# Kernel tuning notes

Hardware: AMD Instinct MI355X
Metric: run time of the kernel (lower is better)

Reference implementation:

```python
import jax, jax.numpy as jnp
import numpy as np

# ---- MUSIC hyperparameters (from init_kwargs) ----
N_FFT = 512
HOP = 256
FS = 16000
F_LOW = 400
F_HIGH = 1000
D_INTER = 0.1
C_SOUND = 343.0
SOURCE_NUM = 2
MIC_NUM = 4
RESOLUTION = 0.01
EST_NUM = 4      # snapshots used for spatial covariance
T_START = 120    # starting STFT frame
EPS = 1e-8
N_SAMPLES = 9_600_000

# sqrt of periodic Hann window (torch.hann_window(512).pow(0.5))
_WIN = np.sqrt(0.5 * (1.0 - np.cos(2.0 * np.pi * np.arange(N_FFT) / N_FFT))).astype(np.float32)
# analog frequency grid and static usable-bin mask
_F_ALL = np.linspace(0.0, FS / 2.0, N_FFT // 2 + 1)
_F_MASK = (_F_ALL >= F_LOW) & (_F_ALL < F_HIGH)
_F_USE = _F_ALL[_F_MASK].astype(np.float32)          # (F_use,) ~ 19 bins
_N_ANGLES = int(180 / RESOLUTION + 1)                 # 18001


def setup_inputs() -> dict:
    key = jax.random.key(0)
    x = jax.random.normal(key, (N_SAMPLES, MIC_NUM), dtype=jnp.float32)
    return {"x": x}


def _music(x):
    # x: (T_samples, C) -> multichannel STFT, center=True reflect pad (torch.stft default)
    xc = x.T                                              # (C, T)
    pad = jnp.pad(xc, ((0, 0), (N_FFT // 2, N_FFT // 2)), mode="reflect")
    n_frames = 1 + x.shape[0] // HOP
    idx = np.arange(n_frames)[:, None] * HOP + np.arange(N_FFT)  # (Tf, 512)
    frames = pad[:, idx] * jnp.asarray(_WIN)              # (C, Tf, 512)
    X = jnp.fft.rfft(frames, axis=-1)                     # (C, Tf, 257) complex64
    X = X[:, :, _F_MASK]                                  # (C, Tf, F_use)

    # spatial covariance from EST_NUM snapshots starting at T_START
    Xs = X[:, T_START:T_START + EST_NUM, :]               # (C, est, F)
    spt = jnp.einsum("ctf,dtf->fcd", Xs, jnp.conj(Xs)) / EST_NUM  # (F, C, C) Hermitian

    # noise subspace: eigenvectors of the MIC_NUM - SOURCE_NUM smallest eigenvalues
    _, V = jnp.linalg.eigh(spt)                           # ascending eigenvalues
    En = V[:, :, : MIC_NUM - SOURCE_NUM]                  # (F, C, K)

    # steering vectors for all angles at once (vectorized over the 18001-angle loop)
    theta = jnp.deg2rad(jnp.linspace(-90.0, 90.0, _N_ANGLES))
    sin_t = jnp.sin(theta).astype(jnp.float32)            # (A,)
    mic_idx = jnp.arange(MIC_NUM, dtype=jnp.float32)      # (C,)
    f_use = jnp.asarray(_F_USE)                           # (F,)
    phase = (2.0 * jnp.pi * D_INTER / C_SOUND) * sin_t[:, None, None] \
            * f_use[None, :, None] * mic_idx[None, None, :]        # (A, F, C)
    steer = jnp.exp(-1j * phase)                          # (A, F, C) complex64

    # project onto noise subspace: MUSIC pseudo-spectrum
    proj = jnp.einsum("afc,fck->afk", steer, En)          # (A, F, K)
    denom = jnp.sum(jnp.abs(proj) ** 2, axis=-1) + EPS    # (A, F)
    spt_spec = jnp.mean(1.0 / denom, axis=1)              # mean over freqs -> (A,)
    return spt_spec


def reference(x):
    return _music(x)
```

## Files before the change

kernel.cpp:

```cpp
#include <hip/hip_runtime.h>
#include <math.h>

#define HOP 256
#define T_START 120
#define NFREQ 19
#define KMIN 13
#define NANGLES 18001

__constant__ double C8[8] = {1.0, 0.70710678118654752, 0.0, -0.70710678118654752,
                             -1.0, -0.70710678118654752, 0.0, 0.70710678118654752};
__constant__ double S8[8] = {0.0, 0.70710678118654752, 1.0, 0.70710678118654752,
                             0.0, -0.70710678118654752, -1.0, -0.70710678118654752};

__global__ __launch_bounds__(64) void k_dft(const float4* __restrict__ x4,
                                            double* __restrict__ ws) {
    const int blk  = blockIdx.x;
    const int k    = blk >> 2;
    const int t    = blk & 3;
    const int lane = threadIdx.x;
    const int kact = KMIN + k;
    const int base = (T_START - 1 + t) * HOP;

    const double cw8 = 0.92387953251128675613;
    const double sw8 = 0.38268343236508977173;
    double sw, cw;
    sincospi((double)lane / 512.0, &sw, &cw);

    double sp, cp;
    sincospi((double)(kact * lane) / 256.0, &sp, &cp);
    const int m = kact & 7;
    const double cd = C8[m], sd = S8[m];

    double xr0 = 0, xi0 = 0, xr1 = 0, xi1 = 0;
    double xr2 = 0, xi2 = 0, xr3 = 0, xi3 = 0;
#pragma unroll
    for (int j = 0; j < 8; ++j) {
        const float4 v = x4[base + lane + 64 * j];
        const double wr = sw * cp;
        const double wi = sw * sp;
        xr0 += (double)v.x * wr;  xi0 -= (double)v.x * wi;
        xr1 += (double)v.y * wr;  xi1 -= (double)v.y * wi;
        xr2 += (double)v.z * wr;  xi2 -= (double)v.z * wi;
        xr3 += (double)v.w * wr;  xi3 -= (double)v.w * wi;
        const double nw = sw * cw8 + cw * sw8;
        cw = cw * cw8 - sw * sw8;
        sw = nw;
        const double np = sp * cd + cp * sd;
        cp = cp * cd - sp * sd;
        sp = np;
    }
#pragma unroll
    for (int off = 32; off > 0; off >>= 1) {
        xr0 += __shfl_down(xr0, off, 64);  xi0 += __shfl_down(xi0, off, 64);
        xr1 += __shfl_down(xr1, off, 64);  xi1 += __shfl_down(xi1, off, 64);
        xr2 += __shfl_down(xr2, off, 64);  xi2 += __shfl_down(xi2, off, 64);
        xr3 += __shfl_down(xr3, off, 64);  xi3 += __shfl_down(xi3, off, 64);
    }
    if (lane == 0) {
        const int idx = k * 16 + t * 4;
        ws[2 * (idx + 0)] = xr0;  ws[2 * (idx + 0) + 1] = xi0;
        ws[2 * (idx + 1)] = xr1;  ws[2 * (idx + 1) + 1] = xi1;
        ws[2 * (idx + 2)] = xr2;  ws[2 * (idx + 2) + 1] = xi2;
        ws[2 * (idx + 3)] = xr3;  ws[2 * (idx + 3) + 1] = xi3;
    }
}

__global__ __launch_bounds__(256, 1) void k_eig_scan(const double* __restrict__ wsX,
                                                     float* __restrict__ out) {
    __shared__ double tb[NFREQ * 7];
    const int tid = threadIdx.x;
    const int i   = blockIdx.x * 256 + tid;

    const double deg = -90.0 + 0.01 * (double)i;
    const double sth = sin(deg * (M_PI / 180.0));
    const double KC  = 2.0 * M_PI * 0.1 / 343.0;
    const double a   = KC * sth;
    double c0, s0, cd, sd;
    sincos(a * (31.25 * (double)KMIN), &s0, &c0);
    sincos(a * 31.25, &sd, &cd);

    if (tid < NFREQ) {
        const int f = tid;
        double Xr[4][4], Xi[4][4];
#pragma unroll
        for (int t = 0; t < 4; ++t)
#pragma unroll
            for (int c = 0; c < 4; ++c) {
                const int idx = f * 16 + t * 4 + c;
                Xr[t][c] = wsX[2 * idx];
                Xi[t][c] = wsX[2 * idx + 1];
            }

        double Ar[4][4], Ai[4][4], Vr[4][4], Vi[4][4];
#pragma unroll
        for (int aa = 0; aa < 4; ++aa)
#pragma unroll
            for (int dd = 0; dd < 4; ++dd) {
                double ar = 0.0, ai = 0.0;
#pragma unroll
                for (int t = 0; t < 4; ++t) {
                    ar += Xr[t][aa] * Xr[t][dd] + Xi[t][aa] * Xi[t][dd];
                    ai += Xi[t][aa] * Xr[t][dd] - Xr[t][aa] * Xi[t][dd];
                }
                Ar[aa][dd] = 0.25 * ar;
                Ai[aa][dd] = 0.25 * ai;
                Vr[aa][dd] = (aa == dd) ? 1.0 : 0.0;
                Vi[aa][dd] = 0.0;
            }

        const int PP[6] = {0, 2, 0, 1, 0, 1};
        const int QQ[6] = {1, 3, 2, 3, 3, 2};
        for (int sweep = 0; sweep < 5; ++sweep) {
#pragma unroll
            for (int r6 = 0; r6 < 6; ++r6) {
                const int p = PP[r6], q = QQ[r6];
                const double zr = Ar[p][q], zi = Ai[p][q];
                const double rr = sqrt(zr * zr + zi * zi);
                if (rr < 1e-30) continue;
                const double tau = (Ar[q][q] - Ar[p][p]) / (2.0 * rr);
                const double sq  = sqrt(tau * tau + 1.0);
                const double tt  = (tau >= 0.0) ? (-1.0 / (tau + sq)) : (1.0 / (sq - tau));
                const double cc  = 1.0 / sqrt(1.0 + tt * tt);
                const double sg  = tt * cc;
                const double inv_r = 1.0 / rr;
                const double sr =  sg * zr * inv_r;
                const double si = -sg * zi * inv_r;
#pragma unroll
                for (int kk = 0; kk < 4; ++kk) {
                    const double apr = Ar[kk][p], api = Ai[kk][p];
                    const double aqr = Ar[kk][q], aqi = Ai[kk][q];
                    Ar[kk][p] = cc * apr + sr * aqr - si * aqi;
                    Ai[kk][p] = cc * api + sr * aqi + si * aqr;
                    Ar[kk][q] = cc * aqr - (sr * apr + si * api);
                    Ai[kk][q] = cc * aqi - (sr * api - si * apr);
                }
#pragma unroll
                for (int kk = 0; kk < 4; ++kk) {
                    const double apr = Ar[p][kk], api = Ai[p][kk];
                    const double aqr = Ar[q][kk], aqi = Ai[q][kk];
                    Ar[p][kk] = cc * apr + sr * aqr + si * aqi;
                    Ai[p][kk] = cc * api + sr * aqi - si * aqr;
                    Ar[q][kk] = cc * aqr - (sr * apr - si * api);
                    Ai[q][kk] = cc * aqi - (sr * api + si * apr);
                }
#pragma unroll
                for (int kk = 0; kk < 4; ++kk) {
                    const double vpr = Vr[kk][p], vpi = Vi[kk][p];
                    const double vqr = Vr[kk][q], vqi = Vi[kk][q];
                    Vr[kk][p] = cc * vpr + sr * vqr - si * vqi;
                    Vi[kk][p] = cc * vpi + sr * vqi + si * vqr;
                    Vr[kk][q] = cc * vqr - (sr * vpr + si * vpi);
                    Vi[kk][q] = cc * vqi - (sr * vpi - si * vpr);
                }
            }
        }

        double dg[4] = {Ar[0][0], Ar[1][1], Ar[2][2], Ar[3][3]};
        int i0 = 0;
#pragma unroll
        for (int j = 1; j < 4; ++j)
            if (dg[j] < dg[i0]) i0 = j;
        int i1 = (i0 == 0) ? 1 : 0;
#pragma unroll
        for (int j = 0; j < 4; ++j)
            if (j != i0 && dg[j] < dg[i1]) i1 = j;

        double u0r[4], u0i[4], u1r[4], u1i[4];
#pragma unroll
        for (int c = 0; c < 4; ++c) {
            u0r[c] = Vr[c][i0]; u0i[c] = Vi[c][i0];
            u1r[c] = Vr[c][i1]; u1i[c] = Vi[c][i1];
        }

        double T0 = 0.0;
#pragma unroll
        for (int c = 0; c < 4; ++c)
            T0 += u0r[c] * u0r[c] + u0i[c] * u0i[c] + u1r[c] * u1r[c] + u1i[c] * u1i[c];
        double q1r = 0, q1i = 0, q2r = 0, q2i = 0, q3r = 0, q3i = 0;
#pragma unroll
        for (int c = 0; c < 3; ++c) {
            q1r += u0r[c] * u0r[c+1] + u0i[c] * u0i[c+1] + u1r[c] * u1r[c+1] + u1i[c] * u1i[c+1];
            q1i += u0i[c] * u0r[c+1] - u0r[c] * u0i[c+1] + u1i[c] * u1r[c+1] - u1r[c] * u1i[c+1];
        }
#pragma unroll
        for (int c = 0; c < 2; ++c) {
            q2r += u0r[c] * u0r[c+2] + u0i[c] * u0i[c+2] + u1r[c] * u1r[c+2] + u1i[c] * u1i[c+2];
            q2i += u0i[c] * u0r[c+2] - u0r[c] * u0i[c+2] + u1i[c] * u1r[c+2] - u1r[c] * u1i[c+2];
        }
        q3r = u0r[0] * u0r[3] + u0i[0] * u0i[3] + u1r[0] * u1r[3] + u1i[0] * u1i[3];
        q3i = u0i[0] * u0r[3] - u0r[0] * u0i[3] + u1i[0] * u1r[3] - u1r[0] * u1i[3];

        double* o = &tb[f * 7];
        o[0] = T0;
        o[1] = q1r; o[2] = q1i;
        o[3] = q2r; o[4] = q2i;
        o[5] = q3r; o[6] = q3i;
    }
    __syncthreads();

    if (i < NANGLES) {
        double sum = 0.0;
        double c = c0, s = s0;
#pragma unroll
        for (int k = 0; k < NFREQ; ++k) {
            const double* e = &tb[7 * k];
            const double c2 = c * c - s * s, s2 = 2.0 * c * s;
            const double c3 = c2 * c - s2 * s, s3 = s2 * c + c2 * s;
            const double den = e[0]
                + 2.0 * (e[1] * c - e[2] * s + e[3] * c2 - e[4] * s2 + e[5] * c3 - e[6] * s3)
                + 1e-8;
            sum += 1.0 / den;
            const double cn = c * cd - s * sd;
            s = s * cd + c * sd;
            c = cn;
        }
        out[i] = (float)(sum * (1.0 / 19.0));
    }
}

extern "C" void kernel_launch(void* const* d_in, const int* in_sizes, int n_in,
                              void* d_out, int out_size, void* d_ws, size_t ws_size,
                              hipStream_t stream) {
    const float4* x4 = (const float4*)d_in[0];
    double* ws = (double*)d_ws;
    float* out = (float*)d_out;

    hipLaunchKernelGGL(k_dft, dim3(NFREQ * 4), dim3(64), 0, stream, x4, ws);
    hipLaunchKernelGGL(k_eig_scan, dim3((NANGLES + 255) / 256), dim3(256), 0, stream,
                       ws, out);
}
```

Measured before the change: 209.0 us.

## Fuse DFT and eigen-scan kernels into one cooperative launch with grid sync

```diff
diff --git a/kernel.cpp b/kernel.cpp
--- a/kernel.cpp
+++ b/kernel.cpp
@@ -1,72 +1,24 @@
 #include <hip/hip_runtime.h>
+#include <hip/hip_cooperative_groups.h>
 #include <math.h>
+
+namespace cg = cooperative_groups;
 
 #define HOP 256
 #define T_START 120
 #define NFREQ 19
 #define KMIN 13
 #define NANGLES 18001
+#define NBLK 71
 
 __constant__ double C8[8] = {1.0, 0.70710678118654752, 0.0, -0.70710678118654752,
                              -1.0, -0.70710678118654752, 0.0, 0.70710678118654752};
 __constant__ double S8[8] = {0.0, 0.70710678118654752, 1.0, 0.70710678118654752,
                              0.0, -0.70710678118654752, -1.0, -0.70710678118654752};
 
-__global__ __launch_bounds__(64) void k_dft(const float4* __restrict__ x4,
-                                            double* __restrict__ ws) {
-    const int blk  = blockIdx.x;
-    const int k    = blk >> 2;
-    const int t    = blk & 3;
-    const int lane = threadIdx.x;
-    const int kact = KMIN + k;
-    const int base = (T_START - 1 + t) * HOP;
-
-    const double cw8 = 0.92387953251128675613;
-    const double sw8 = 0.38268343236508977173;
-    double sw, cw;
-    sincospi((double)lane / 512.0, &sw, &cw);
-
-    double sp, cp;
-    sincospi((double)(kact * lane) / 256.0, &sp, &cp);
-    const int m = kact & 7;
-    const double cd = C8[m], sd = S8[m];
-
-    double xr0 = 0, xi0 = 0, xr1 = 0, xi1 = 0;
-    double xr2 = 0, xi2 = 0, xr3 = 0, xi3 = 0;
-#pragma unroll
-    for (int j = 0; j < 8; ++j) {
-        const float4 v = x4[base + lane + 64 * j];
-        const double wr = sw * cp;
-        const double wi = sw * sp;
-        xr0 += (double)v.x * wr;  xi0 -= (double)v.x * wi;
-        xr1 += (double)v.y * wr;  xi1 -= (double)v.y * wi;
-        xr2 += (double)v.z * wr;  xi2 -= (double)v.z * wi;
-        xr3 += (double)v.w * wr;  xi3 -= (double)v.w * wi;
-        const double nw = sw * cw8 + cw * sw8;
-        cw = cw * cw8 - sw * sw8;
-        sw = nw;
-        const double np = sp * cd + cp * sd;
-        cp = cp * cd - sp * sd;
-        sp = np;
-    }
-#pragma unroll
-    for (int off = 32; off > 0; off >>= 1) {
-        xr0 += __shfl_down(xr0, off, 64);  xi0 += __shfl_down(xi0, off, 64);
-        xr1 += __shfl_down(xr1, off, 64);  xi1 += __shfl_down(xi1, off, 64);
-        xr2 += __shfl_down(xr2, off, 64);  xi2 += __shfl_down(xi2, off, 64);
-        xr3 += __shfl_down(xr3, off, 64);  xi3 += __shfl_down(xi3, off, 64);
-    }
-    if (lane == 0) {
-        const int idx = k * 16 + t * 4;
-        ws[2 * (idx + 0)] = xr0;  ws[2 * (idx + 0) + 1] = xi0;
-        ws[2 * (idx + 1)] = xr1;  ws[2 * (idx + 1) + 1] = xi1;
-        ws[2 * (idx + 2)] = xr2;  ws[2 * (idx + 2) + 1] = xi2;
-        ws[2 * (idx + 3)] = xr3;  ws[2 * (idx + 3) + 1] = xi3;
-    }
-}
-
-__global__ __launch_bounds__(256, 1) void k_eig_scan(const double* __restrict__ wsX,
-                                                     float* __restrict__ out) {
+__global__ __launch_bounds__(256, 1) void k_all(const float4* __restrict__ x4,
+                                                double* __restrict__ ws,
+                                                float* __restrict__ out) {
     __shared__ double tb[NFREQ * 7];
     const int tid = threadIdx.x;
     const int i   = blockIdx.x * 256 + tid;
@@ -79,7 +31,63 @@
     sincos(a * (31.25 * (double)KMIN), &s0, &c0);
     sincos(a * 31.25, &sd, &cd);
 
+    const int wid = (blockIdx.x << 2) + (tid >> 6);
+    if (wid < NFREQ * 4) {
+        const int k    = wid >> 2;
+        const int t    = wid & 3;
+        const int lane = tid & 63;
+        const int kact = KMIN + k;
+        const int base = (T_START - 1 + t) * HOP;
+
+        const double cw8 = 0.92387953251128675613;
+        const double sw8 = 0.38268343236508977173;
+        double sw, cw;
+        sincospi((double)lane / 512.0, &sw, &cw);
+
+        double sp, cp;
+        sincospi((double)(kact * lane) / 256.0, &sp, &cp);
+        const int m = kact & 7;
+        const double cdp = C8[m], sdp = S8[m];
+
+        double xr0 = 0, xi0 = 0, xr1 = 0, xi1 = 0;
+        double xr2 = 0, xi2 = 0, xr3 = 0, xi3 = 0;
+#pragma unroll
+        for (int j = 0; j < 8; ++j) {
+            const float4 v = x4[base + lane + 64 * j];
+            const double wr = sw * cp;
+            const double wi = sw * sp;
+            xr0 += (double)v.x * wr;  xi0 -= (double)v.x * wi;
+            xr1 += (double)v.y * wr;  xi1 -= (double)v.y * wi;
+            xr2 += (double)v.z * wr;  xi2 -= (double)v.z * wi;
+            xr3 += (double)v.w * wr;  xi3 -= (double)v.w * wi;
+            const double nw = sw * cw8 + cw * sw8;
+            cw = cw * cw8 - sw * sw8;
+            sw = nw;
+            const double np = sp * cdp + cp * sdp;
+            cp = cp * cdp - sp * sdp;
+            sp = np;
+        }
+#pragma unroll
+        for (int off = 32; off > 0; off >>= 1) {
+            xr0 += __shfl_down(xr0, off, 64);  xi0 += __shfl_down(xi0, off, 64);
+            xr1 += __shfl_down(xr1, off, 64);  xi1 += __shfl_down(xi1, off, 64);
+            xr2 += __shfl_down(xr2, off, 64);  xi2 += __shfl_down(xi2, off, 64);
+            xr3 += __shfl_down(xr3, off, 64);  xi3 += __shfl_down(xi3, off, 64);
+        }
+        if (lane == 0) {
+            const int idx = k * 16 + t * 4;
+            ws[2 * (idx + 0)] = xr0;  ws[2 * (idx + 0) + 1] = xi0;
+            ws[2 * (idx + 1)] = xr1;  ws[2 * (idx + 1) + 1] = xi1;
+            ws[2 * (idx + 2)] = xr2;  ws[2 * (idx + 2) + 1] = xi2;
+            ws[2 * (idx + 3)] = xr3;  ws[2 * (idx + 3) + 1] = xi3;
+        }
+        __threadfence();
+    }
+
+    cg::this_grid().sync();
+
     if (tid < NFREQ) {
+        __threadfence();
         const int f = tid;
         double Xr[4][4], Xi[4][4];
 #pragma unroll
@@ -87,8 +95,8 @@
 #pragma unroll
             for (int c = 0; c < 4; ++c) {
                 const int idx = f * 16 + t * 4 + c;
-                Xr[t][c] = wsX[2 * idx];
-                Xi[t][c] = wsX[2 * idx + 1];
+                Xr[t][c] = ws[2 * idx];
+                Xi[t][c] = ws[2 * idx + 1];
             }
 
         double Ar[4][4], Ai[4][4], Vr[4][4], Vi[4][4];
@@ -225,7 +233,7 @@
     double* ws = (double*)d_ws;
     float* out = (float*)d_out;
 
-    hipLaunchKernelGGL(k_dft, dim3(NFREQ * 4), dim3(64), 0, stream, x4, ws);
-    hipLaunchKernelGGL(k_eig_scan, dim3((NANGLES + 255) / 256), dim3(256), 0, stream,
-                       ws, out);
+    void* args[] = {(void*)&x4, (void*)&ws, (void*)&out};
+    hipLaunchCooperativeKernel(reinterpret_cast<void*>(k_all), dim3(NBLK), dim3(256),
+                               args, 0, stream);
 }
```

Measured after the change: 236.9 us. 13.3% more time.
